# Optimization experiments

Measured on AMD Instinct MI355X. Metric: run time of the kernel, lower is better.

## Reference

```python
import jax, jax.numpy as jnp
import numpy as np

N_NODES, N_EDGES, B, L = 20000, 320000, 64, 48
EMB, OUT, HEADS, HID = 256, 64, 4, 512
S_DIM, R_DIM = 64, 64
TIME_NUM, CAT_NUM = 48, 201


def lrelu(x, s=0.2):
    return jnp.where(x >= 0, x, s * x)


def gru_cell(x, h, Wi, Wh, bi, bh):
    # PyTorch GRUCell math
    gi = x @ Wi.T + bi
    gh = h @ Wh.T + bh
    ir, iz, ig = jnp.split(gi, 3, axis=-1)
    hr, hz, hg = jnp.split(gh, 3, axis=-1)
    r = jax.nn.sigmoid(ir + hr)
    z = jax.nn.sigmoid(iz + hz)
    n = jnp.tanh(ig + r * hg)
    return (1.0 - z) * n + z * h


def gru_seq(x, Wi, Wh, bi, bh, reverse=False):
    # x: [B,L,D] -> [B,L,H]
    xs = jnp.swapaxes(x, 0, 1)
    if reverse:
        xs = xs[::-1]
    h0 = jnp.zeros((x.shape[0], Wh.shape[1]), x.dtype)

    def step(h, xt):
        h2 = gru_cell(xt, h, Wi, Wh, bi, bh)
        return h2, h2

    _, ys = jax.lax.scan(step, h0, xs)
    if reverse:
        ys = ys[::-1]
    return jnp.swapaxes(ys, 0, 1)


def setup_inputs() -> dict:
    key = jax.random.key(0)
    ks = iter(jax.random.split(key, 64))
    f32 = jnp.float32

    def rn(shape, s=0.1):
        return (s * jax.random.normal(next(ks), shape)).astype(f32)

    inp = {
        'graph_x': jnp.arange(N_NODES),
        'edge_index': jax.random.randint(next(ks), (2, N_EDGES), 0, N_NODES),
        'edge_attr': jax.random.uniform(next(ks), (N_EDGES,), f32),
        'batch_x': jax.random.randint(next(ks), (B, L), 0, N_NODES),
        'batch_time': jax.random.randint(next(ks), (B, L), 0, TIME_NUM),
        'batch_cat': jax.random.randint(next(ks), (B, L), 0, CAT_NUM),
        'poi_time': jax.random.randint(next(ks), (N_NODES,), 0, TIME_NUM),
        'poi_cat': jax.random.randint(next(ks), (N_NODES,), 0, CAT_NUM),
        # params
        'node_emb': rn((N_NODES, EMB), 1.0),
        'W_gat': rn((EMB, HEADS * OUT), 0.05),
        'att_src': rn((HEADS, OUT), 0.05),
        'att_dst': rn((HEADS, OUT), 0.05),
        'gat_bias': rn((HEADS * OUT,)),
        'time_table': rn((TIME_NUM, EMB), 1.0),
        'cat_table': rn((CAT_NUM, EMB), 1.0),
        'W_w': rn((EMB, 3 * EMB)), 'b_w': rn((EMB,)),
        'Wi_f': rn((3 * HID, EMB), 0.05), 'Wh_f': rn((3 * HID, HID), 0.05),
        'bi_f': jnp.zeros((3 * HID,), f32), 'bh_f': jnp.zeros((3 * HID,), f32),
        'Wi_bw': rn((3 * HID, EMB), 0.05), 'Wh_bw': rn((3 * HID, HID), 0.05),
        'bi_bw': jnp.zeros((3 * HID,), f32), 'bh_bw': jnp.zeros((3 * HID,), f32),
        'Wi_u': rn((3 * HID, 2 * HID), 0.05), 'Wh_u': rn((3 * HID, HID), 0.05),
        'bi_u': jnp.zeros((3 * HID,), f32), 'bh_u': jnp.zeros((3 * HID,), f32),
        'Ws_m': rn((S_DIM, 2 * HID)), 'bs_m': rn((S_DIM,)),
        'Ws_lv': rn((S_DIM, 2 * HID)), 'bs_lv': rn((S_DIM,)),
        'Wr_m': rn((R_DIM, HID)), 'br_m': rn((R_DIM,)),
        'Wr_lv': rn((R_DIM, HID)), 'br_lv': rn((R_DIM,)),
        'Wp1_i': rn((3 * HID, R_DIM), 0.05), 'Wp1_h': rn((3 * HID, HID), 0.05),
        'bp1_i': jnp.zeros((3 * HID,), f32), 'bp1_h': jnp.zeros((3 * HID,), f32),
        'Wp2_i': rn((3 * HID, HID), 0.05), 'Wp2_h': rn((3 * HID, HID), 0.05),
        'bp2_i': jnp.zeros((3 * HID,), f32), 'bp2_h': jnp.zeros((3 * HID,), f32),
        'Wpm': rn((R_DIM, HID)), 'bpm': rn((R_DIM,)),
        'Wplv': rn((R_DIM, HID)), 'bplv': rn((R_DIM,)),
        'Wd': rn((N_NODES, S_DIM + R_DIM)), 'bd': rn((N_NODES,)),
    }
    return inp


def forward(graph_x, edge_index, edge_attr, batch_x, batch_time, batch_cat,
            poi_time, poi_cat, node_emb, W_gat, att_src, att_dst, gat_bias,
            time_table, cat_table, W_w, b_w, Wi_f, Wh_f, bi_f, bh_f,
            Wi_bw, Wh_bw, bi_bw, bh_bw, Wi_u, Wh_u, bi_u, bh_u,
            Ws_m, bs_m, Ws_lv, bs_lv, Wr_m, br_m, Wr_lv, br_lv,
            Wp1_i, Wp1_h, bp1_i, bp1_h, Wp2_i, Wp2_h, bp2_i, bp2_h,
            Wpm, bpm, Wplv, bplv, Wd, bd):
    Bn, Ln = batch_x.shape
    N = node_emb.shape[0]
    heads, C = att_src.shape

    # --- weighted GAT layer over the POI graph ---
    h = node_emb[graph_x]                                   # [N, EMB]
    xW = (h @ W_gat).reshape(N, heads, C)                   # [N, H, C]
    src, dst = edge_index[0], edge_index[1]
    e = lrelu((xW * att_src).sum(-1)[src] + (xW * att_dst).sum(-1)[dst])  # [E, H]
    emax = jax.ops.segment_max(e, dst, num_segments=N)
    a = jnp.exp(e - emax[dst])
    asum = jax.ops.segment_sum(a, dst, num_segments=N)
    att = a / (asum[dst] + 1e-16)
    msg = (att * edge_attr[:, None])[:, :, None] * xW[src]  # [E, H, C]
    p = jax.ops.segment_sum(msg, dst, num_segments=N).reshape(N, heads * C) + gat_bias

    # --- per-step feature build ---
    p_h = p[batch_x]                                        # [B, L, EMB]
    t_e = time_table[batch_time]
    c_e = cat_table[batch_cat]
    ph = jnp.concatenate([p_h, t_e, c_e], axis=2) @ W_w.T + b_w  # [B, L, EMB]

    # --- posterior encode: biGRU -> s, uniGRU -> r ---
    f_fwd = gru_seq(ph, Wi_f, Wh_f, bi_f, bh_f)
    f_bwd = gru_seq(ph, Wi_bw, Wh_bw, bi_bw, bh_bw, reverse=True)
    features = jnp.concatenate([f_fwd, f_bwd], axis=2)      # [B, L, 2H]
    Hh = Wh_f.shape[1]
    frontal = features[:, Ln - 1, :Hh]
    backward = features[:, 0, Hh:2 * Hh]
    g = jnp.concatenate([frontal, backward], axis=1)
    s_mean = lrelu(g @ Ws_m.T + bs_m)
    s_logvar = lrelu(g @ Ws_lv.T + bs_lv)

    key = jax.random.key(42)
    k1, k2, k3 = jax.random.split(key, 3)
    s_post = s_mean + jax.random.normal(k1, s_mean.shape, s_mean.dtype) * jnp.exp(0.5 * s_logvar)

    r_feat = gru_seq(features, Wi_u, Wh_u, bi_u, bh_u)      # [B, L, H]
    r_mean = r_feat @ Wr_m.T + br_m
    r_logvar = r_feat @ Wr_lv.T + br_lv
    r_post = r_mean + jax.random.normal(k2, r_mean.shape, r_mean.dtype) * jnp.exp(0.5 * r_logvar)

    # --- prior: 2-layer GRUCell unroll fed with shifted r_post ---
    Rd = r_post.shape[2]
    r_in = jnp.concatenate([jnp.zeros((Bn, 1, Rd), r_post.dtype), r_post[:, :-1]], axis=1)
    r_in_t = jnp.swapaxes(r_in, 0, 1)                       # [L, B, R]
    eps = jax.random.normal(k3, (Ln, Bn, Rd), r_post.dtype)

    def pstep(carry, xe):
        h1, h2 = carry
        rt, ep = xe
        h1 = gru_cell(rt, h1, Wp1_i, Wp1_h, bp1_i, bp1_h)
        h2 = gru_cell(h1, h2, Wp2_i, Wp2_h, bp2_i, bp2_h)
        mt = h2 @ Wpm.T + bpm
        lvt = h2 @ Wplv.T + bplv
        rp = mt + ep * jnp.exp(0.5 * lvt)
        return (h1, h2), (mt, lvt, rp)

    h10 = jnp.zeros((Bn, Hh), r_post.dtype)
    h20 = jnp.zeros((Bn, Hh), r_post.dtype)
    _, (ms, lvs, rps) = jax.lax.scan(pstep, (h10, h20), (r_in_t, eps))
    r_mean_prior = jnp.swapaxes(ms, 0, 1)
    r_logvar_prior = jnp.swapaxes(lvs, 0, 1)
    r_prior = jnp.swapaxes(rps, 0, 1)

    # --- decode ---
    s_expand = jnp.broadcast_to(s_post[:, None, :], (Bn, Ln, s_post.shape[1]))
    zf = jnp.concatenate([r_post, s_expand], axis=2)
    recon_x = zf @ Wd.T + bd                                # [B, L, node_num]
    return (s_mean, s_logvar, s_post, r_mean, r_logvar, r_post,
            r_mean_prior, r_logvar_prior, r_prior, recon_x)


def reference(graph_x, edge_index, edge_attr, batch_x, batch_time, batch_cat,
              poi_time, poi_cat, node_emb, W_gat, att_src, att_dst, gat_bias,
              time_table, cat_table, W_w, b_w, Wi_f, Wh_f, bi_f, bh_f,
              Wi_bw, Wh_bw, bi_bw, bh_bw, Wi_u, Wh_u, bi_u, bh_u,
              Ws_m, bs_m, Ws_lv, bs_lv, Wr_m, br_m, Wr_lv, br_lv,
              Wp1_i, Wp1_h, bp1_i, bp1_h, Wp2_i, Wp2_h, bp2_i, bp2_h,
              Wpm, bpm, Wplv, bplv, Wd, bd):
    return forward(graph_x, edge_index, edge_attr, batch_x, batch_time, batch_cat,
                   poi_time, poi_cat, node_emb, W_gat, att_src, att_dst, gat_bias,
                   time_table, cat_table, W_w, b_w, Wi_f, Wh_f, bi_f, bh_f,
                   Wi_bw, Wh_bw, bi_bw, bh_bw, Wi_u, Wh_u, bi_u, bh_u,
                   Ws_m, bs_m, Ws_lv, bs_lv, Wr_m, br_m, Wr_lv, br_lv,
                   Wp1_i, Wp1_h, bp1_i, bp1_h, Wp2_i, Wp2_h, bp2_i, bp2_h,
                   Wpm, bpm, Wplv, bplv, Wd, bd)
```

## Files before the change

kernel.cpp:

```cpp
#include <hip/hip_runtime.h>
#include <stdint.h>
#include <stddef.h>

#define DEV __device__ __forceinline__

typedef float f32x4 __attribute__((ext_vector_type(4)));

__host__ __device__ inline void tf2x32(uint32_t k0, uint32_t k1,
                                       uint32_t x0, uint32_t x1,
                                       uint32_t* o0, uint32_t* o1) {
  uint32_t ks2 = k0 ^ k1 ^ 0x1BD11BDAu;
  uint32_t ks[3] = {k0, k1, ks2};
  x0 += k0; x1 += k1;
  const uint32_t R[8] = {13u,15u,26u,6u,17u,29u,16u,24u};
  for (int r = 0; r < 5; ++r) {
    const uint32_t* rot = (r & 1) ? (R + 4) : R;
    for (int i = 0; i < 4; ++i) {
      x0 += x1;
      uint32_t d = rot[i];
      x1 = (x1 << d) | (x1 >> (32u - d));
      x1 ^= x0;
    }
    x0 += ks[(r + 1) % 3];
    x1 += ks[(r + 2) % 3] + (uint32_t)(r + 1);
  }
  *o0 = x0; *o1 = x1;
}

DEV float erfinv_approx(float x) {
  float w = -logf((1.0f - x) * (1.0f + x));
  float p;
  if (w < 5.0f) {
    w = w - 2.5f;
    p = 2.81022636e-08f;
    p = fmaf(p, w, 3.43273939e-07f);
    p = fmaf(p, w, -3.5233877e-06f);
    p = fmaf(p, w, -4.39150654e-06f);
    p = fmaf(p, w, 0.00021858087f);
    p = fmaf(p, w, -0.00125372503f);
    p = fmaf(p, w, -0.00417768164f);
    p = fmaf(p, w, 0.246640727f);
    p = fmaf(p, w, 1.50140941f);
  } else {
    w = sqrtf(w) - 3.0f;
    p = -0.000200214257f;
    p = fmaf(p, w, 0.000100950558f);
    p = fmaf(p, w, 0.00134934322f);
    p = fmaf(p, w, -0.00367342844f);
    p = fmaf(p, w, 0.00573950773f);
    p = fmaf(p, w, -0.0076224613f);
    p = fmaf(p, w, 0.00943887047f);
    p = fmaf(p, w, 1.00167406f);
    p = fmaf(p, w, 2.83297682f);
  }
  return p * x;
}

DEV float normal_part(uint32_t ka, uint32_t kb, uint32_t idx) {
  uint32_t b1, b2;
  tf2x32(ka, kb, 0u, idx, &b1, &b2);
  uint32_t bits = b1 ^ b2;
  float f = __uint_as_float((bits >> 9) | 0x3f800000u) - 1.0f;
  const float lo = -0.99999994f;
  float u = f * 2.0f + lo;
  u = fmaxf(lo, u);
  return 1.41421356f * erfinv_approx(u);
}

DEV float lrelu(float x) { return x >= 0.f ? x : 0.2f * x; }
DEV float sigm(float x) { return 1.0f / (1.0f + expf(-x)); }

DEV float gru_out(float ir, float iz, float ig, float hr, float hz, float hg, float hprev) {
  float r = sigm(ir + hr);
  float z = sigm(iz + hz);
  float n = tanhf(ig + r * hg);
  return (1.0f - z) * n + z * hprev;
}

DEV float dot4f(float4 a, float4 b, float acc) {
  return fmaf(a.x, b.x, fmaf(a.y, b.y, fmaf(a.z, b.z, fmaf(a.w, b.w, acc))));
}

template <int K4>
DEV void dot2(const float* __restrict__ h, const float* __restrict__ w0,
              const float* __restrict__ w1, float& a0, float& a1) {
  const float4* h4 = (const float4*)h;
  const float4* p0 = (const float4*)w0;
  const float4* p1 = (const float4*)w1;
  #pragma unroll 4
  for (int k = 0; k < K4; ++k) {
    float4 hv = h4[k];
    float4 v0 = p0[k], v1 = p1[k];
    a0 = dot4f(hv, v0, a0);
    a1 = dot4f(hv, v1, a1);
  }
}

template <int K4>
DEV void dotT3p(const float* __restrict__ hp, int b,
                const float* __restrict__ w0, const float* __restrict__ w1,
                const float* __restrict__ w2, float& a0, float& a1, float& a2) {
  const float4* __restrict__ w04 = (const float4*)w0;
  const float4* __restrict__ w14 = (const float4*)w1;
  const float4* __restrict__ w24 = (const float4*)w2;
  const float4* __restrict__ h4 = (const float4*)hp;
  #pragma unroll
  for (int k4 = 0; k4 < K4; ++k4) {
    float4 hv = h4[k4 * 64 + b];
    a0 = dot4f(w04[k4], hv, a0);
    a1 = dot4f(w14[k4], hv, a1);
    a2 = dot4f(w24[k4], hv, a2);
  }
}

template <int K4>
DEV void dotT3_lds(const float* __restrict__ hl, int b,
                   const float* __restrict__ w0, const float* __restrict__ w1,
                   const float* __restrict__ w2, float& a0, float& a1, float& a2) {
  const float4* __restrict__ h4 = (const float4*)hl;
  const float4* __restrict__ w04 = (const float4*)w0;
  const float4* __restrict__ w14 = (const float4*)w1;
  const float4* __restrict__ w24 = (const float4*)w2;
  #pragma unroll 8
  for (int k4 = 0; k4 < K4; ++k4) {
    float4 hv = h4[k4 * 64 + b];
    a0 = dot4f(w04[k4], hv, a0);
    a1 = dot4f(w14[k4], hv, a1);
    a2 = dot4f(w24[k4], hv, a2);
  }
}

template <int N16>
DEV void stage_lds(float* __restrict__ dst, const float* __restrict__ src) {
  const float4* __restrict__ s4 = (const float4*)src;
  float4* __restrict__ d4 = (float4*)dst;
  int tid = threadIdx.x;
  constexpr int CH = (N16 < 16) ? N16 : 16;
  #pragma unroll
  for (int r = 0; r < N16; r += CH) {
    float4 v[CH];
    #pragma unroll
    for (int u = 0; u < CH; ++u) v[u] = s4[(size_t)(r + u) * 256 + tid];
    #pragma unroll
    for (int u = 0; u < CH; ++u) d4[(size_t)(r + u) * 256 + tid] = v[u];
  }
}

DEV size_t pk(int k, int b) { return (size_t)(k >> 2) * 256 + b * 4 + (k & 3); }

DEV void coh_store_i(int* p, int v) {
  asm volatile("global_store_dword %0, %1, off sc0 sc1" :: "v"(p), "v"(v) : "memory");
}
DEV void coh_store_f(float* p, float v) {
  asm volatile("global_store_dword %0, %1, off sc0 sc1" :: "v"(p), "v"(v) : "memory");
}
DEV void coh_store_f4(float* p, f32x4 v) {
  asm volatile("global_store_dwordx4 %0, %1, off sc0 sc1" :: "v"(p), "v"(v) : "memory");
}
DEV int coh_load_i(const int* p) {
  int v;
  asm volatile("global_load_dword %0, %1, off sc0 sc1\n\ts_waitcnt vmcnt(0)"
               : "=v"(v) : "v"(p) : "memory");
  return v;
}

DEV void flag_barrier(int* __restrict__ flags, int nblk, int myidx, int gen) {
  asm volatile("s_waitcnt vmcnt(0)" ::: "memory");
  __syncthreads();
  if (threadIdx.x == 0) coh_store_i(flags + myidx, gen);
  if ((int)threadIdx.x < nblk) {
    int spins = 0;
    while (coh_load_i(flags + threadIdx.x) < gen) {
      __builtin_amdgcn_s_sleep(2);
      if (++spins > (1 << 22)) break;
    }
  }
  __syncthreads();
}

DEV void wait_group(const int* __restrict__ flags, int nblk, int thr) {
  if ((int)threadIdx.x < nblk) {
    int spins = 0;
    while (coh_load_i(flags + threadIdx.x) < thr) {
      __builtin_amdgcn_s_sleep(2);
      if (++spins > (1 << 22)) break;
    }
  }
  __syncthreads();
}

DEV void store_packed_tile4(float* dst_t, const float (*smem)[64], int j0) {
  if (threadIdx.x < 64) {
    int bb = threadIdx.x;
    f32x4 v;
    v.x = smem[0][bb];
    v.y = smem[1][bb];
    v.z = smem[2][bb];
    v.w = smem[3][bb];
    coh_store_f4(dst_t + (size_t)(j0 >> 2) * 256 + bb * 4, v);
  }
}

#define GBM 128
#define GBN 128
#define GBK 16

__global__ __launch_bounds__(256) void gemm_nt(
    const float* __restrict__ A, const float* __restrict__ Bt,
    const float* __restrict__ bias, float* __restrict__ C,
    int M, int N, int K, const int* __restrict__ gatherA, int trGI) {
  __shared__ float As[GBK][GBM + 4];
  __shared__ float Bs[GBK][GBN + 4];
  const int bm = blockIdx.y * GBM;
  const int bn = blockIdx.x * GBN;
  const int tid = threadIdx.x;
  const int tx = tid & 15;
  const int ty = tid >> 4;
  float acc[8][8];
  #pragma unroll
  for (int i = 0; i < 8; ++i)
    #pragma unroll
    for (int j = 0; j < 8; ++j) acc[i][j] = 0.f;

  for (int k0 = 0; k0 < K; k0 += GBK) {
    #pragma unroll
    for (int s = 0; s < 2; ++s) {
      int f = tid + s * 256;
      int r = f >> 2, kq = f & 3;
      int row = bm + r;
      float4 v = make_float4(0.f, 0.f, 0.f, 0.f);
      if (row < M) {
        int ar = gatherA ? gatherA[row] : row;
        v = *(const float4*)&A[(size_t)ar * K + k0 + kq * 4];
      }
      As[kq * 4 + 0][r] = v.x;
      As[kq * 4 + 1][r] = v.y;
      As[kq * 4 + 2][r] = v.z;
      As[kq * 4 + 3][r] = v.w;
    }
    #pragma unroll
    for (int s = 0; s < 2; ++s) {
      int f = tid + s * 256;
      int r = f >> 2, kq = f & 3;
      int col = bn + r;
      float4 v = make_float4(0.f, 0.f, 0.f, 0.f);
      if (col < N) v = *(const float4*)&Bt[(size_t)col * K + k0 + kq * 4];
      Bs[kq * 4 + 0][r] = v.x;
      Bs[kq * 4 + 1][r] = v.y;
      Bs[kq * 4 + 2][r] = v.z;
      Bs[kq * 4 + 3][r] = v.w;
    }
    __syncthreads();
    #pragma unroll
    for (int kk = 0; kk < GBK; ++kk) {
      float4 a0 = *(const float4*)&As[kk][ty * 4];
      float4 a1 = *(const float4*)&As[kk][64 + ty * 4];
      float4 b0 = *(const float4*)&Bs[kk][tx * 4];
      float4 b1 = *(const float4*)&Bs[kk][64 + tx * 4];
      float av[8] = {a0.x, a0.y, a0.z, a0.w, a1.x, a1.y, a1.z, a1.w};
      float bv[8] = {b0.x, b0.y, b0.z, b0.w, b1.x, b1.y, b1.z, b1.w};
      #pragma unroll
      for (int i = 0; i < 8; ++i)
        #pragma unroll
        for (int j = 0; j < 8; ++j)
          acc[i][j] = fmaf(av[i], bv[j], acc[i][j]);
    }
    __syncthreads();
  }
  #pragma unroll
  for (int i = 0; i < 8; ++i) {
    int row = bm + ((i < 4) ? (ty * 4 + i) : (64 + ty * 4 + i - 4));
    if (row >= M) continue;
    if (trGI) {
      #pragma unroll
      for (int j = 0; j < 8; ++j) {
        int col = bn + ((j < 4) ? (tx * 4 + j) : (64 + tx * 4 + j - 4));
        if (col >= N) continue;
        float v = acc[i][j] + (bias ? bias[col] : 0.f);
        int bb = row / 48, tt = row - bb * 48;
        C[((size_t)tt * N + col) * 64 + bb] = v;
      }
    } else {
      #pragma unroll
      for (int g = 0; g < 2; ++g) {
        int col0 = bn + g * 64 + tx * 4;
        if (col0 + 3 >= N) continue;
        float4 v;
        v.x = acc[i][g * 4 + 0] + (bias ? bias[col0 + 0] : 0.f);
        v.y = acc[i][g * 4 + 1] + (bias ? bias[col0 + 1] : 0.f);
        v.z = acc[i][g * 4 + 2] + (bias ? bias[col0 + 2] : 0.f);
        v.w = acc[i][g * 4 + 3] + (bias ? bias[col0 + 3] : 0.f);
        *(float4*)&C[(size_t)row * N + col0] = v;
      }
    }
  }
}

__global__ void k_transpose(const float* __restrict__ W, float* __restrict__ Wt,
                            int rows, int cols) {
  int idx = blockIdx.x * 256 + threadIdx.x;
  if (idx >= rows * cols) return;
  int r = idx / cols, c = idx % cols;
  Wt[(size_t)c * rows + r] = W[idx];
}

__global__ void k_count_deg(const int* __restrict__ dst, int* __restrict__ deg, int nE) {
  int e = blockIdx.x * 256 + threadIdx.x;
  if (e < nE) atomicAdd(&deg[dst[e]], 1);
}

__global__ __launch_bounds__(1024) void k_scan(const int* __restrict__ deg,
                                               int* __restrict__ off,
                                               int* __restrict__ cursor, int n) {
  __shared__ int tmp[1024];
  __shared__ int carry_s;
  if (threadIdx.x == 0) carry_s = 0;
  __syncthreads();
  for (int base = 0; base < n; base += 1024) {
    int i = base + (int)threadIdx.x;
    int v = (i < n) ? deg[i] : 0;
    tmp[threadIdx.x] = v;
    __syncthreads();
    for (int s = 1; s < 1024; s <<= 1) {
      int t = (threadIdx.x >= (unsigned)s) ? tmp[threadIdx.x - s] : 0;
      __syncthreads();
      tmp[threadIdx.x] += t;
      __syncthreads();
    }
    int incl = tmp[threadIdx.x];
    int base_c = carry_s;
    int excl = incl - v;
    if (i < n) { off[i] = base_c + excl; cursor[i] = base_c + excl; }
    __syncthreads();
    if (threadIdx.x == 1023) carry_s = base_c + incl;
    __syncthreads();
  }
  if (threadIdx.x == 0) off[n] = carry_s;
}

__global__ void k_scatter(const int* __restrict__ dst, int* __restrict__ cursor,
                          int* __restrict__ csr, int nE) {
  int e = blockIdx.x * 256 + threadIdx.x;
  if (e < nE) {
    int pos = atomicAdd(&cursor[dst[e]], 1);
    csr[pos] = e;
  }
}

__global__ void k_alpha(const float* __restrict__ xW, const float* __restrict__ att_src,
                        const float* __restrict__ att_dst, float* __restrict__ as_,
                        float* __restrict__ ad_) {
  int i = blockIdx.x * 256 + threadIdx.x;
  if (i >= 80000) return;
  int n = i >> 2, h = i & 3;
  const float* xr = xW + (size_t)n * 256 + h * 64;
  const float* s = att_src + h * 64;
  const float* d = att_dst + h * 64;
  float a = 0.f, b = 0.f;
  dot2<16>(xr, s, d, a, b);
  as_[i] = a;
  ad_[i] = b;
}

__global__ __launch_bounds__(256) void k_gat_node(
    const float* __restrict__ xW, const float* __restrict__ as_,
    const float* __restrict__ ad_, const int* __restrict__ off,
    const int* __restrict__ csr, const int* __restrict__ esrc,
    const float* __restrict__ eattr, const float* __restrict__ gat_bias,
    float* __restrict__ p) {
  int n = blockIdx.x;
  int h = threadIdx.x >> 6;
  int c = threadIdx.x & 63;
  int s0 = off[n], s1 = off[n + 1];
  float adn = ad_[n * 4 + h];
  float m = -3.0e38f;
  for (int idx = s0; idx < s1; ++idx) {
    int e = csr[idx];
    int s = esrc[e];
    float ev = lrelu(as_[s * 4 + h] + adn);
    m = fmaxf(m, ev);
  }
  float sum = 0.f;
  for (int idx = s0; idx < s1; ++idx) {
    int e = csr[idx];
    int s = esrc[e];
    float ev = lrelu(as_[s * 4 + h] + adn);
    sum += expf(ev - m);
  }
  float acc = 0.f;
  for (int idx = s0; idx < s1; ++idx) {
    int e = csr[idx];
    int s = esrc[e];
    float ev = lrelu(as_[s * 4 + h] + adn);
    float w = expf(ev - m) / (sum + 1e-16f) * eattr[e];
    acc = fmaf(w, xW[(size_t)s * 256 + h * 64 + c], acc);
  }
  p[(size_t)n * 256 + h * 64 + c] = acc + gat_bias[h * 64 + c];
}

__global__ void k_build_X(const float* __restrict__ p, const float* __restrict__ tt,
                          const float* __restrict__ ct, const int* __restrict__ bx,
                          const int* __restrict__ btm, const int* __restrict__ bct,
                          float* __restrict__ X) {
  int idx = blockIdx.x * 256 + threadIdx.x;
  if (idx >= 3072 * 768) return;
  int rl = idx / 768, c = idx % 768;
  float v;
  if (c < 256) v = p[(size_t)bx[rl] * 256 + c];
  else if (c < 512) v = tt[(size_t)btm[rl] * 256 + (c - 256)];
  else v = ct[(size_t)bct[rl] * 256 + (c - 512)];
  X[idx] = v;
}


__global__ __launch_bounds__(256, 1) void k_gru_bidir_fused(
    const float* __restrict__ giT_f, const float* __restrict__ giT_b,
    const float* __restrict__ Wh_f, const float* __restrict__ bh_f,
    const float* __restrict__ Wh_b, const float* __restrict__ bh_b,
    float* __restrict__ features, float* __restrict__ hTb,
    int* __restrict__ flags) {
  __shared__ float lds_h[32768];
  __shared__ float smem[4][64];
  int w = threadIdx.x >> 6;
  int b = threadIdx.x & 63;
  int slot = blockIdx.x * 4 + w;
  int dir = slot >> 9;
  int j = slot & 511;
  int j0 = (blockIdx.x * 4) & 511;
  int gbid = blockIdx.x & 127;
  int* gflags = flags + dir * 128;
  const float* Wh = dir ? Wh_b : Wh_f;
  const float* bh = dir ? bh_b : bh_f;
  const float* gi = dir ? giT_b : giT_f;
  const float* w0 = Wh + (size_t)j * 512;
  const float* w1 = Wh + (size_t)(512 + j) * 512;
  const float* w2 = Wh + (size_t)(1024 + j) * 512;
  float bhr = bh[j], bhz = bh[512 + j], bhg = bh[1024 + j];
  float* hD = hTb + (size_t)dir * 48 * 32768;
  for (int s = 0; s < 48; ++s) {
    int t = dir ? (47 - s) : s;
    const float* gir = gi + (size_t)t * 98304;
    float giv0 = gir[j * 64 + b];
    float giv1 = gir[(512 + j) * 64 + b];
    float giv2 = gir[(1024 + j) * 64 + b];
    float hr = bhr, hz = bhz, hg = bhg, hprev = 0.f;
    if (s > 0) {
      int tp = dir ? (t + 1) : (t - 1);
      stage_lds<32>(lds_h, hD + (size_t)tp * 32768);
      __syncthreads();
      dotT3_lds<128>(lds_h, b, w0, w1, w2, hr, hz, hg);
      hprev = lds_h[pk(j, b)];
    }
    float hnew = gru_out(giv0, giv1, giv2, hr, hz, hg, hprev);
    smem[w][b] = hnew;
    features[((size_t)(b * 48 + t)) * 1024 + dir * 512 + j] = hnew;
    __syncthreads();
    store_packed_tile4(hD + (size_t)t * 32768, smem, j0);
    flag_barrier(gflags, 128, gbid, s + 1);
  }
}

__global__ __launch_bounds__(256, 1) void k_gru_u_fused(
    const float* __restrict__ giT, const float* __restrict__ Wh,
    const float* __restrict__ bh, float* __restrict__ r_feat,
    float* __restrict__ hU, int* __restrict__ flags) {
  __shared__ float lds_h[32768];
  __shared__ float smem[4][64];
  int w = threadIdx.x >> 6;
  int b = threadIdx.x & 63;
  int j = blockIdx.x * 4 + w;
  int j0 = blockIdx.x * 4;
  const float* w0 = Wh + (size_t)j * 512;
  const float* w1 = Wh + (size_t)(512 + j) * 512;
  const float* w2 = Wh + (size_t)(1024 + j) * 512;
  float bhr = bh[j], bhz = bh[512 + j], bhg = bh[1024 + j];
  for (int s = 0; s < 48; ++s) {
    const float* gir = giT + (size_t)s * 98304;
    float giv0 = gir[j * 64 + b];
    float giv1 = gir[(512 + j) * 64 + b];
    float giv2 = gir[(1024 + j) * 64 + b];
    float hr = bhr, hz = bhz, hg = bhg, hprev = 0.f;
    if (s > 0) {
      stage_lds<32>(lds_h, hU + (size_t)(s - 1) * 32768);
      __syncthreads();
      dotT3_lds<128>(lds_h, b, w0, w1, w2, hr, hz, hg);
      hprev = lds_h[pk(j, b)];
    }
    float hnew = gru_out(giv0, giv1, giv2, hr, hz, hg, hprev);
    smem[w][b] = hnew;
    r_feat[((size_t)(b * 48 + s)) * 512 + j] = hnew;
    __syncthreads();
    store_packed_tile4(hU + (size_t)s * 32768, smem, j0);
    flag_barrier(flags, 128, blockIdx.x, s + 1);
  }
}

__global__ __launch_bounds__(256, 1) void k_prior_fused(
    const float* __restrict__ r_post,
    const float* __restrict__ Wp1_i, const float* __restrict__ Wp1_h,
    const float* __restrict__ bp1_i, const float* __restrict__ bp1_h,
    const float* __restrict__ Wp2_i, const float* __restrict__ Wp2_h,
    const float* __restrict__ bp2_i, const float* __restrict__ bp2_h,
    float* __restrict__ h1S, float* __restrict__ h2S,
    float* __restrict__ rT, int* __restrict__ flags) {
  __shared__ float lds_h[32768];
  __shared__ float smem[4][64];
  int w = threadIdx.x >> 6;
  int b = threadIdx.x & 63;
  int cell = blockIdx.x >> 7;
  int gbid = blockIdx.x & 127;
  int slot = blockIdx.x * 4 + w;
  int j = slot & 511;
  int j0 = (blockIdx.x * 4) & 511;
  int* flagsA = flags;
  int* flagsB = flags + 128;

  if (cell == 0) {
    int tid = gbid * 256 + threadIdx.x;
    for (int x = tid; x < 48 * 64 * 64; x += 32768) {
      int b0 = x & 63;
      int i0 = (x >> 6) & 63;
      int t0 = x >> 12;
      coh_store_f(rT + (size_t)t0 * 4096 + pk(i0, b0),
                  r_post[((size_t)(b0 * 48 + t0)) * 64 + i0]);
    }
    flag_barrier(flagsA, 128, gbid, 1);

    const float* wi0 = Wp1_i + (size_t)j * 64;
    const float* wi1 = Wp1_i + (size_t)(512 + j) * 64;
    const float* wi2 = Wp1_i + (size_t)(1024 + j) * 64;
    const float* wh0 = Wp1_h + (size_t)j * 512;
    const float* wh1 = Wp1_h + (size_t)(512 + j) * 512;
    const float* wh2 = Wp1_h + (size_t)(1024 + j) * 512;
    float bir = bp1_i[j], biz = bp1_i[512 + j], big = bp1_i[1024 + j];
    float bhr = bp1_h[j], bhz = bp1_h[512 + j], bhg = bp1_h[1024 + j];
    for (int k = 0; k < 48; ++k) {
      float ir = bir, iz = biz, ig = big;
      float hr = bhr, hz = bhz, hg = bhg, hprev = 0.f;
      if (k > 0) {
        stage_lds<32>(lds_h, h1S + (size_t)(k - 1) * 32768);
        dotT3p<16>(rT + (size_t)(k - 1) * 4096, b, wi0, wi1, wi2, ir, iz, ig);
        __syncthreads();
        dotT3_lds<128>(lds_h, b, wh0, wh1, wh2, hr, hz, hg);
        hprev = lds_h[pk(j, b)];
      }
      smem[w][b] = gru_out(ir, iz, ig, hr, hz, hg, hprev);
      __syncthreads();
      store_packed_tile4(h1S + (size_t)k * 32768, smem, j0);
      flag_barrier(flagsA, 128, gbid, k + 2);
    }
  } else {
    const float* wi0 = Wp2_i + (size_t)j * 512;
    const float* wi1 = Wp2_i + (size_t)(512 + j) * 512;
    const float* wi2 = Wp2_i + (size_t)(1024 + j) * 512;
    const float* wh0 = Wp2_h + (size_t)j * 512;
    const float* wh1 = Wp2_h + (size_t)(512 + j) * 512;
    const float* wh2 = Wp2_h + (size_t)(1024 + j) * 512;
    float bir = bp2_i[j], biz = bp2_i[512 + j], big = bp2_i[1024 + j];
    float bhr = bp2_h[j], bhz = bp2_h[512 + j], bhg = bp2_h[1024 + j];
    for (int t = 0; t < 48; ++t) {
      wait_group(flagsA, 128, t + 2);
      stage_lds<32>(lds_h, h1S + (size_t)t * 32768);
      __syncthreads();
      float ir = bir, iz = biz, ig = big;
      dotT3_lds<128>(lds_h, b, wi0, wi1, wi2, ir, iz, ig);
      float hr = bhr, hz = bhz, hg = bhg, hprev = 0.f;
      if (t > 0) {
        __syncthreads();
        stage_lds<32>(lds_h, h2S + (size_t)(t - 1) * 32768);
        __syncthreads();
        dotT3_lds<128>(lds_h, b, wh0, wh1, wh2, hr, hz, hg);
        hprev = lds_h[pk(j, b)];
      }
      smem[w][b] = gru_out(ir, iz, ig, hr, hz, hg, hprev);
      __syncthreads();
      store_packed_tile4(h2S + (size_t)t * 32768, smem, j0);
      flag_barrier(flagsB, 128, gbid, t + 1);
    }
  }
}

__global__ void k_s_head(const float* __restrict__ features,
                         const float* __restrict__ Ws_m, const float* __restrict__ bs_m,
                         const float* __restrict__ Ws_lv, const float* __restrict__ bs_lv,
                         float* __restrict__ out, uint32_t ka, uint32_t kb) {
  int idx = blockIdx.x * 256 + threadIdx.x;
  if (idx >= 4096) return;
  int i = idx & 63, b = idx >> 6;
  const float* fr = features + ((size_t)(b * 48 + 47)) * 1024;
  const float* bk = features + ((size_t)(b * 48 + 0)) * 1024 + 512;
  const float* wm = Ws_m + (size_t)i * 1024;
  const float* wl = Ws_lv + (size_t)i * 1024;
  float m = 0.f, lv = 0.f;
  dot2<128>(fr, wm, wl, m, lv);
  dot2<128>(bk, wm + 512, wl + 512, m, lv);
  m = lrelu(m + bs_m[i]);
  lv = lrelu(lv + bs_lv[i]);
  float nz = normal_part(ka, kb, (uint32_t)idx);
  out[idx] = m;
  out[4096 + idx] = lv;
  out[8192 + idx] = m + nz * expf(0.5f * lv);
}

__global__ void k_r_head(const float* __restrict__ r_feat,
                         const float* __restrict__ Wr_m, const float* __restrict__ br_m,
                         const float* __restrict__ Wr_lv, const float* __restrict__ br_lv,
                         float* __restrict__ out, uint32_t ka, uint32_t kb) {
  int idx = blockIdx.x * 256 + threadIdx.x;
  if (idx >= 196608) return;
  int i = idx & 63;
  int bt = idx >> 6;
  const float* f = r_feat + (size_t)bt * 512;
  float m = 0.f, lv = 0.f;
  dot2<128>(f, Wr_m + (size_t)i * 512, Wr_lv + (size_t)i * 512, m, lv);
  m += br_m[i];
  lv += br_lv[i];
  float nz = normal_part(ka, kb, (uint32_t)idx);
  out[12288 + idx] = m;
  out[208896 + idx] = lv;
  out[405504 + idx] = m + nz * expf(0.5f * lv);
}

__global__ void k_prior_out(const float* __restrict__ h2S,
                            const float* __restrict__ Wpm, const float* __restrict__ bpm,
                            const float* __restrict__ Wplv, const float* __restrict__ bplv,
                            float* __restrict__ out, uint32_t ka, uint32_t kb) {
  int idx = blockIdx.x * 256 + threadIdx.x;
  if (idx >= 196608) return;
  int i = idx & 63;
  int bt = idx >> 6;
  int b = bt & 63;
  int t = bt >> 6;
  const float4* h4 = (const float4*)(h2S + (size_t)t * 32768);
  const float4* wm4 = (const float4*)(Wpm + (size_t)i * 512);
  const float4* wl4 = (const float4*)(Wplv + (size_t)i * 512);
  float m = 0.f, lv = 0.f;
  #pragma unroll 8
  for (int k4 = 0; k4 < 128; ++k4) {
    float4 hv = h4[k4 * 64 + b];
    m = dot4f(wm4[k4], hv, m);
    lv = dot4f(wl4[k4], hv, lv);
  }
  m += bpm[i];
  lv += bplv[i];
  float ep = normal_part(ka, kb, (uint32_t)idx);
  float rp = m + ep * expf(0.5f * lv);
  size_t o = ((size_t)b * 48 + t) * 64 + i;
  out[602112 + o] = m;
  out[798720 + o] = lv;
  out[995328 + o] = rp;
}

__global__ void k_build_zf(const float* __restrict__ out, float* __restrict__ zf) {
  int idx = blockIdx.x * 256 + threadIdx.x;
  if (idx >= 3072 * 128) return;
  int row = idx >> 7, c = idx & 127;
  float v;
  if (c < 64) v = out[405504 + row * 64 + c];
  else v = out[8192 + (row / 48) * 64 + (c - 64)];
  zf[idx] = v;
}

extern "C" void kernel_launch(void* const* d_in, const int* in_sizes, int n_in,
                              void* d_out, int out_size, void* d_ws, size_t ws_size,
                              hipStream_t stream) {
  const int* graph_x = (const int*)d_in[0];
  const int* edge_index = (const int*)d_in[1];
  const float* edge_attr = (const float*)d_in[2];
  const int* batch_x = (const int*)d_in[3];
  const int* batch_time = (const int*)d_in[4];
  const int* batch_cat = (const int*)d_in[5];
  const float* node_emb = (const float*)d_in[8];
  const float* W_gat = (const float*)d_in[9];
  const float* att_src = (const float*)d_in[10];
  const float* att_dst = (const float*)d_in[11];
  const float* gat_bias = (const float*)d_in[12];
  const float* time_table = (const float*)d_in[13];
  const float* cat_table = (const float*)d_in[14];
  const float* W_w = (const float*)d_in[15];
  const float* b_w = (const float*)d_in[16];
  const float* Wi_f = (const float*)d_in[17];
  const float* Wh_f = (const float*)d_in[18];
  const float* bi_f = (const float*)d_in[19];
  const float* bh_f = (const float*)d_in[20];
  const float* Wi_bw = (const float*)d_in[21];
  const float* Wh_bw = (const float*)d_in[22];
  const float* bi_bw = (const float*)d_in[23];
  const float* bh_bw = (const float*)d_in[24];
  const float* Wi_u = (const float*)d_in[25];
  const float* Wh_u = (const float*)d_in[26];
  const float* bi_u = (const float*)d_in[27];
  const float* bh_u = (const float*)d_in[28];
  const float* Ws_m = (const float*)d_in[29];
  const float* bs_m = (const float*)d_in[30];
  const float* Ws_lv = (const float*)d_in[31];
  const float* bs_lv = (const float*)d_in[32];
  const float* Wr_m = (const float*)d_in[33];
  const float* br_m = (const float*)d_in[34];
  const float* Wr_lv = (const float*)d_in[35];
  const float* br_lv = (const float*)d_in[36];
  const float* Wp1_i = (const float*)d_in[37];
  const float* Wp1_h = (const float*)d_in[38];
  const float* bp1_i = (const float*)d_in[39];
  const float* bp1_h = (const float*)d_in[40];
  const float* Wp2_i = (const float*)d_in[41];
  const float* Wp2_h = (const float*)d_in[42];
  const float* bp2_i = (const float*)d_in[43];
  const float* bp2_h = (const float*)d_in[44];
  const float* Wpm = (const float*)d_in[45];
  const float* bpm = (const float*)d_in[46];
  const float* Wplv = (const float*)d_in[47];
  const float* bplv = (const float*)d_in[48];
  const float* Wd = (const float*)d_in[49];
  const float* bd = (const float*)d_in[50];
  float* out = (float*)d_out;

  uint32_t k1a, k1b, k2a, k2b, k3a, k3b;
  tf2x32(0u, 42u, 0u, 0u, &k1a, &k1b);
  tf2x32(0u, 42u, 0u, 1u, &k2a, &k2b);
  tf2x32(0u, 42u, 0u, 2u, &k3a, &k3b);

  float* ws = (float*)d_ws;
  size_t o = 0;
  auto alloc = [&](size_t n) { float* q = ws + o; o += n; return q; };
  float* R1 = alloc(5120000);
  float* R2 = alloc(5120000);
  float* R3 = alloc(4718592);
  float* R4 = alloc(786432);
  float* as_ = alloc(80000);
  float* ad_ = alloc(80000);
  float* Wgt = alloc(65536);
  int* deg = (int*)alloc(20000);
  int* off = (int*)alloc(20001);
  int* cursor = (int*)alloc(20000);
  int* csr = (int*)alloc(320000);
  float* rT = alloc(196608);
  int* flags = (int*)alloc(768);

  float* xW = R1;
  float* features = R1;
  float* r_feat = R1 + 3145728;
  float* p = R2;
  float* giT_b = R2;
  float* hU = R2;
  float* X = R3;
  float* giT_f = R3;
  float* giT_u = R3;
  float* h1S = R3;
  float* h2S = R3 + 1572864;
  float* ph = R4;
  float* zf = R4;
  float* hTb = out + 1191936;

  const int* esrc = edge_index;
  const int* edst = edge_index + 320000;

  dim3 B(256);

  (void)hipMemsetAsync(deg, 0, 20000 * sizeof(int), stream);
  (void)hipMemsetAsync(flags, 0, 768 * sizeof(int), stream);

  k_transpose<<<dim3(256), B, 0, stream>>>(W_gat, Wgt, 256, 256);
  k_count_deg<<<dim3(1250), B, 0, stream>>>(edst, deg, 320000);
  k_scan<<<dim3(1), dim3(1024), 0, stream>>>(deg, off, cursor, 20000);
  k_scatter<<<dim3(1250), B, 0, stream>>>(edst, cursor, csr, 320000);
  gemm_nt<<<dim3(2, 157), B, 0, stream>>>(node_emb, Wgt, nullptr, xW,
                                          20000, 256, 256, graph_x, 0);
  k_alpha<<<dim3(313), B, 0, stream>>>(xW, att_src, att_dst, as_, ad_);
  k_gat_node<<<dim3(20000), B, 0, stream>>>(xW, as_, ad_, off, csr, esrc,
                                            edge_attr, gat_bias, p);

  k_build_X<<<dim3(9216), B, 0, stream>>>(p, time_table, cat_table, batch_x,
                                          batch_time, batch_cat, X);
  gemm_nt<<<dim3(2, 24), B, 0, stream>>>(X, W_w, b_w, ph, 3072, 256, 768,
                                         nullptr, 0);

  gemm_nt<<<dim3(12, 24), B, 0, stream>>>(ph, Wi_f, bi_f, giT_f, 3072, 1536, 256,
                                          nullptr, 1);
  gemm_nt<<<dim3(12, 24), B, 0, stream>>>(ph, Wi_bw, bi_bw, giT_b, 3072, 1536, 256,
                                          nullptr, 1);
  k_gru_bidir_fused<<<dim3(256), B, 0, stream>>>(
      giT_f, giT_b, Wh_f, bh_f, Wh_bw, bh_bw, features, hTb, flags);

  k_s_head<<<dim3(16), B, 0, stream>>>(features, Ws_m, bs_m, Ws_lv, bs_lv,
                                       out, k1a, k1b);

  gemm_nt<<<dim3(12, 24), B, 0, stream>>>(features, Wi_u, bi_u, giT_u,
                                          3072, 1536, 1024, nullptr, 1);
  k_gru_u_fused<<<dim3(128), B, 0, stream>>>(giT_u, Wh_u, bh_u, r_feat,
                                             hU, flags + 256);

  k_r_head<<<dim3(768), B, 0, stream>>>(r_feat, Wr_m, br_m, Wr_lv, br_lv,
                                        out, k2a, k2b);

  k_prior_fused<<<dim3(256), B, 0, stream>>>(
      out + 405504, Wp1_i, Wp1_h, bp1_i, bp1_h, Wp2_i, Wp2_h, bp2_i, bp2_h,
      h1S, h2S, rT, flags + 384);
  k_prior_out<<<dim3(768), B, 0, stream>>>(h2S, Wpm, bpm, Wplv, bplv,
                                           out, k3a, k3b);

  k_build_zf<<<dim3(1536), B, 0, stream>>>(out, zf);
  gemm_nt<<<dim3(157, 24), B, 0, stream>>>(zf, Wd, bd, out + 1191936,
                                           3072, 20000, 128, nullptr, 0);
}
```

Measured before the change: 5.108 ms.

## Restructure prior GRU kernel into batch-grouped tiles with group-local flag barriers

The two-cell prior GRU kernel is rewritten. Each block now handles 32 hidden units by 4 batch rows, with the K reduction split across two halves and combined through shared memory. Each block stages only a 4-row hidden tile instead of the full 64x512 state, and the grid-wide barrier over 128 blocks becomes a barrier among 16 blocks that share a batch group. The r_post transpose moves into a separate pre-kernel, and the output head reads the new batch-major layout. The intent is to cut LDS staging cost and barrier latency per timestep and to allow two blocks per CU. The cost is that weights are re-read by 16 batch groups and there are more per-step syncthreads.

```diff
diff --git a/kernel.cpp b/kernel.cpp
--- a/kernel.cpp
+++ b/kernel.cpp
@@ -97,23 +97,6 @@
 }
 
 template <int K4>
-DEV void dotT3p(const float* __restrict__ hp, int b,
-                const float* __restrict__ w0, const float* __restrict__ w1,
-                const float* __restrict__ w2, float& a0, float& a1, float& a2) {
-  const float4* __restrict__ w04 = (const float4*)w0;
-  const float4* __restrict__ w14 = (const float4*)w1;
-  const float4* __restrict__ w24 = (const float4*)w2;
-  const float4* __restrict__ h4 = (const float4*)hp;
-  #pragma unroll
-  for (int k4 = 0; k4 < K4; ++k4) {
-    float4 hv = h4[k4 * 64 + b];
-    a0 = dot4f(w04[k4], hv, a0);
-    a1 = dot4f(w14[k4], hv, a1);
-    a2 = dot4f(w24[k4], hv, a2);
-  }
-}
-
-template <int K4>
 DEV void dotT3_lds(const float* __restrict__ hl, int b,
                    const float* __restrict__ w0, const float* __restrict__ w1,
                    const float* __restrict__ w2, float& a0, float& a1, float& a2) {
@@ -411,7 +394,6 @@
   else v = ct[(size_t)bct[rl] * 256 + (c - 512)];
   X[idx] = v;
 }
-
 
 __global__ __launch_bounds__(256, 1) void k_gru_bidir_fused(
     const float* __restrict__ giT_f, const float* __restrict__ giT_b,
@@ -495,87 +477,162 @@
   }
 }
 
-__global__ __launch_bounds__(256, 1) void k_prior_fused(
-    const float* __restrict__ r_post,
+
+__global__ void k_prior_pre(const float* __restrict__ r_post,
+                            float* __restrict__ rTP) {
+  int idx = blockIdx.x * 256 + threadIdx.x;
+  if (idx >= 196608) return;
+  int i = idx & 63;
+  int rest = idx >> 6;
+  int bl = rest & 3;
+  int bg = (rest >> 2) & 15;
+  int t = rest >> 6;
+  rTP[idx] = r_post[((size_t)((bg * 4 + bl) * 48 + t)) * 64 + i];
+}
+
+__global__ __launch_bounds__(256, 2) void k_prior2(
+    const float* __restrict__ rTP,
     const float* __restrict__ Wp1_i, const float* __restrict__ Wp1_h,
     const float* __restrict__ bp1_i, const float* __restrict__ bp1_h,
     const float* __restrict__ Wp2_i, const float* __restrict__ Wp2_h,
     const float* __restrict__ bp2_i, const float* __restrict__ bp2_h,
-    float* __restrict__ h1S, float* __restrict__ h2S,
-    float* __restrict__ rT, int* __restrict__ flags) {
-  __shared__ float lds_h[32768];
-  __shared__ float smem[4][64];
-  int w = threadIdx.x >> 6;
-  int b = threadIdx.x & 63;
-  int cell = blockIdx.x >> 7;
-  int gbid = blockIdx.x & 127;
-  int slot = blockIdx.x * 4 + w;
-  int j = slot & 511;
-  int j0 = (blockIdx.x * 4) & 511;
+    float* __restrict__ h1P, float* __restrict__ h2P,
+    int* __restrict__ flags) {
+  __shared__ float lds_h[4][512];
+  __shared__ float part_i[2][128][3];
+  __shared__ float part_h[2][128][3];
+  int bid = blockIdx.x;
+  int cell = bid >> 8;
+  int lid = bid & 255;
+  int jg = lid >> 4, bg = lid & 15;
+  int tid = threadIdx.x;
+  int half = tid >> 7;
+  int c = tid & 127;
+  int jl = c & 31;
+  int bl = c >> 5;
+  int j = jg * 32 + jl;
   int* flagsA = flags;
-  int* flagsB = flags + 128;
+  int* flagsB = flags + 256;
+  float4* d4 = (float4*)&lds_h[0][0];
 
   if (cell == 0) {
-    int tid = gbid * 256 + threadIdx.x;
-    for (int x = tid; x < 48 * 64 * 64; x += 32768) {
-      int b0 = x & 63;
-      int i0 = (x >> 6) & 63;
-      int t0 = x >> 12;
-      coh_store_f(rT + (size_t)t0 * 4096 + pk(i0, b0),
-                  r_post[((size_t)(b0 * 48 + t0)) * 64 + i0]);
-    }
-    flag_barrier(flagsA, 128, gbid, 1);
-
-    const float* wi0 = Wp1_i + (size_t)j * 64;
-    const float* wi1 = Wp1_i + (size_t)(512 + j) * 64;
-    const float* wi2 = Wp1_i + (size_t)(1024 + j) * 64;
-    const float* wh0 = Wp1_h + (size_t)j * 512;
-    const float* wh1 = Wp1_h + (size_t)(512 + j) * 512;
-    const float* wh2 = Wp1_h + (size_t)(1024 + j) * 512;
-    float bir = bp1_i[j], biz = bp1_i[512 + j], big = bp1_i[1024 + j];
-    float bhr = bp1_h[j], bhz = bp1_h[512 + j], bhg = bp1_h[1024 + j];
+    const float4* wi0 = (const float4*)(Wp1_i + (size_t)j * 64);
+    const float4* wi1 = (const float4*)(Wp1_i + (size_t)(512 + j) * 64);
+    const float4* wi2 = (const float4*)(Wp1_i + (size_t)(1024 + j) * 64);
+    const float4* wh0 = (const float4*)(Wp1_h + (size_t)j * 512);
+    const float4* wh1 = (const float4*)(Wp1_h + (size_t)(512 + j) * 512);
+    const float4* wh2 = (const float4*)(Wp1_h + (size_t)(1024 + j) * 512);
     for (int k = 0; k < 48; ++k) {
-      float ir = bir, iz = biz, ig = big;
-      float hr = bhr, hz = bhz, hg = bhg, hprev = 0.f;
       if (k > 0) {
-        stage_lds<32>(lds_h, h1S + (size_t)(k - 1) * 32768);
-        dotT3p<16>(rT + (size_t)(k - 1) * 4096, b, wi0, wi1, wi2, ir, iz, ig);
+        const float4* s4 = (const float4*)(h1P + ((size_t)(k - 1) * 16 + bg) * 2048);
+        d4[tid] = s4[tid];
+        d4[tid + 256] = s4[tid + 256];
         __syncthreads();
-        dotT3_lds<128>(lds_h, b, wh0, wh1, wh2, hr, hz, hg);
-        hprev = lds_h[pk(j, b)];
+        const float4* h4 = (const float4*)&lds_h[bl][0];
+        float a0 = 0.f, a1 = 0.f, a2 = 0.f;
+        #pragma unroll 8
+        for (int q = 0; q < 64; ++q) {
+          int k4 = half * 64 + q;
+          float4 hv = h4[k4];
+          a0 = dot4f(wh0[k4], hv, a0);
+          a1 = dot4f(wh1[k4], hv, a1);
+          a2 = dot4f(wh2[k4], hv, a2);
+        }
+        part_h[half][c][0] = a0; part_h[half][c][1] = a1; part_h[half][c][2] = a2;
+        const float4* r4 =
+            (const float4*)(rTP + (((size_t)(k - 1) * 16 + bg) * 4 + bl) * 64);
+        float b0 = 0.f, b1 = 0.f, b2 = 0.f;
+        #pragma unroll
+        for (int q = 0; q < 8; ++q) {
+          int k4 = half * 8 + q;
+          float4 rv = r4[k4];
+          b0 = dot4f(wi0[k4], rv, b0);
+          b1 = dot4f(wi1[k4], rv, b1);
+          b2 = dot4f(wi2[k4], rv, b2);
+        }
+        part_i[half][c][0] = b0; part_i[half][c][1] = b1; part_i[half][c][2] = b2;
+        __syncthreads();
       }
-      smem[w][b] = gru_out(ir, iz, ig, hr, hz, hg, hprev);
+      if (tid < 128) {
+        int cc = tid, jl2 = cc & 31, bl2 = cc >> 5;
+        int jj = jg * 32 + jl2;
+        float ir = bp1_i[jj], iz = bp1_i[512 + jj], ig = bp1_i[1024 + jj];
+        float hr = bp1_h[jj], hz = bp1_h[512 + jj], hg = bp1_h[1024 + jj];
+        float hp = 0.f;
+        if (k > 0) {
+          ir += part_i[0][cc][0] + part_i[1][cc][0];
+          iz += part_i[0][cc][1] + part_i[1][cc][1];
+          ig += part_i[0][cc][2] + part_i[1][cc][2];
+          hr += part_h[0][cc][0] + part_h[1][cc][0];
+          hz += part_h[0][cc][1] + part_h[1][cc][1];
+          hg += part_h[0][cc][2] + part_h[1][cc][2];
+          hp = lds_h[bl2][jj];
+        }
+        coh_store_f(h1P + ((size_t)k * 16 + bg) * 2048 + bl2 * 512 + jj,
+                    gru_out(ir, iz, ig, hr, hz, hg, hp));
+      }
+      flag_barrier(flagsA + bg * 16, 16, jg, k + 1);
+    }
+  } else {
+    const float4* wi0 = (const float4*)(Wp2_i + (size_t)j * 512);
+    const float4* wi1 = (const float4*)(Wp2_i + (size_t)(512 + j) * 512);
+    const float4* wi2 = (const float4*)(Wp2_i + (size_t)(1024 + j) * 512);
+    const float4* wh0 = (const float4*)(Wp2_h + (size_t)j * 512);
+    const float4* wh1 = (const float4*)(Wp2_h + (size_t)(512 + j) * 512);
+    const float4* wh2 = (const float4*)(Wp2_h + (size_t)(1024 + j) * 512);
+    for (int t = 0; t < 48; ++t) {
+      wait_group(flagsA + bg * 16, 16, t + 1);
+      const float4* s4 = (const float4*)(h1P + ((size_t)t * 16 + bg) * 2048);
+      d4[tid] = s4[tid];
+      d4[tid + 256] = s4[tid + 256];
       __syncthreads();
-      store_packed_tile4(h1S + (size_t)k * 32768, smem, j0);
-      flag_barrier(flagsA, 128, gbid, k + 2);
-    }
-  } else {
-    const float* wi0 = Wp2_i + (size_t)j * 512;
-    const float* wi1 = Wp2_i + (size_t)(512 + j) * 512;
-    const float* wi2 = Wp2_i + (size_t)(1024 + j) * 512;
-    const float* wh0 = Wp2_h + (size_t)j * 512;
-    const float* wh1 = Wp2_h + (size_t)(512 + j) * 512;
-    const float* wh2 = Wp2_h + (size_t)(1024 + j) * 512;
-    float bir = bp2_i[j], biz = bp2_i[512 + j], big = bp2_i[1024 + j];
-    float bhr = bp2_h[j], bhz = bp2_h[512 + j], bhg = bp2_h[1024 + j];
-    for (int t = 0; t < 48; ++t) {
-      wait_group(flagsA, 128, t + 2);
-      stage_lds<32>(lds_h, h1S + (size_t)t * 32768);
+      const float4* h4 = (const float4*)&lds_h[bl][0];
+      float b0 = 0.f, b1 = 0.f, b2 = 0.f;
+      #pragma unroll 8
+      for (int q = 0; q < 64; ++q) {
+        int k4 = half * 64 + q;
+        float4 hv = h4[k4];
+        b0 = dot4f(wi0[k4], hv, b0);
+        b1 = dot4f(wi1[k4], hv, b1);
+        b2 = dot4f(wi2[k4], hv, b2);
+      }
+      part_i[half][c][0] = b0; part_i[half][c][1] = b1; part_i[half][c][2] = b2;
       __syncthreads();
-      float ir = bir, iz = biz, ig = big;
-      dotT3_lds<128>(lds_h, b, wi0, wi1, wi2, ir, iz, ig);
-      float hr = bhr, hz = bhz, hg = bhg, hprev = 0.f;
       if (t > 0) {
+        const float4* s4b = (const float4*)(h2P + ((size_t)(t - 1) * 16 + bg) * 2048);
+        d4[tid] = s4b[tid];
+        d4[tid + 256] = s4b[tid + 256];
         __syncthreads();
-        stage_lds<32>(lds_h, h2S + (size_t)(t - 1) * 32768);
+        float a0 = 0.f, a1 = 0.f, a2 = 0.f;
+        #pragma unroll 8
+        for (int q = 0; q < 64; ++q) {
+          int k4 = half * 64 + q;
+          float4 hv = h4[k4];
+          a0 = dot4f(wh0[k4], hv, a0);
+          a1 = dot4f(wh1[k4], hv, a1);
+          a2 = dot4f(wh2[k4], hv, a2);
+        }
+        part_h[half][c][0] = a0; part_h[half][c][1] = a1; part_h[half][c][2] = a2;
         __syncthreads();
-        dotT3_lds<128>(lds_h, b, wh0, wh1, wh2, hr, hz, hg);
-        hprev = lds_h[pk(j, b)];
       }
-      smem[w][b] = gru_out(ir, iz, ig, hr, hz, hg, hprev);
-      __syncthreads();
-      store_packed_tile4(h2S + (size_t)t * 32768, smem, j0);
-      flag_barrier(flagsB, 128, gbid, t + 1);
+      if (tid < 128) {
+        int cc = tid, jl2 = cc & 31, bl2 = cc >> 5;
+        int jj = jg * 32 + jl2;
+        float ir = part_i[0][cc][0] + part_i[1][cc][0] + bp2_i[jj];
+        float iz = part_i[0][cc][1] + part_i[1][cc][1] + bp2_i[512 + jj];
+        float ig = part_i[0][cc][2] + part_i[1][cc][2] + bp2_i[1024 + jj];
+        float hr = bp2_h[jj], hz = bp2_h[512 + jj], hg = bp2_h[1024 + jj];
+        float hp = 0.f;
+        if (t > 0) {
+          hr += part_h[0][cc][0] + part_h[1][cc][0];
+          hz += part_h[0][cc][1] + part_h[1][cc][1];
+          hg += part_h[0][cc][2] + part_h[1][cc][2];
+          hp = lds_h[bl2][jj];
+        }
+        coh_store_f(h2P + ((size_t)t * 16 + bg) * 2048 + bl2 * 512 + jj,
+                    gru_out(ir, iz, ig, hr, hz, hg, hp));
+      }
+      flag_barrier(flagsB + bg * 16, 16, jg, t + 1);
     }
   }
 }
@@ -621,7 +678,7 @@
   out[405504 + idx] = m + nz * expf(0.5f * lv);
 }
 
-__global__ void k_prior_out(const float* __restrict__ h2S,
+__global__ void k_prior_out(const float* __restrict__ h2P,
                             const float* __restrict__ Wpm, const float* __restrict__ bpm,
                             const float* __restrict__ Wplv, const float* __restrict__ bplv,
                             float* __restrict__ out, uint32_t ka, uint32_t kb) {
@@ -631,13 +688,14 @@
   int bt = idx >> 6;
   int b = bt & 63;
   int t = bt >> 6;
-  const float4* h4 = (const float4*)(h2S + (size_t)t * 32768);
+  const float4* h4 =
+      (const float4*)(h2P + (((size_t)t * 16 + (b >> 2)) * 4 + (b & 3)) * 512);
   const float4* wm4 = (const float4*)(Wpm + (size_t)i * 512);
   const float4* wl4 = (const float4*)(Wplv + (size_t)i * 512);
   float m = 0.f, lv = 0.f;
   #pragma unroll 8
   for (int k4 = 0; k4 < 128; ++k4) {
-    float4 hv = h4[k4 * 64 + b];
+    float4 hv = h4[k4];
     m = dot4f(wm4[k4], hv, m);
     lv = dot4f(wl4[k4], hv, lv);
   }
@@ -734,8 +792,8 @@
   int* off = (int*)alloc(20001);
   int* cursor = (int*)alloc(20000);
   int* csr = (int*)alloc(320000);
-  float* rT = alloc(196608);
-  int* flags = (int*)alloc(768);
+  float* rTP = alloc(196608);
+  int* flags = (int*)alloc(1024);
 
   float* xW = R1;
   float* features = R1;
@@ -746,8 +804,8 @@
   float* X = R3;
   float* giT_f = R3;
   float* giT_u = R3;
-  float* h1S = R3;
-  float* h2S = R3 + 1572864;
+  float* h1P = R3;
+  float* h2P = R3 + 1572864;
   float* ph = R4;
   float* zf = R4;
   float* hTb = out + 1191936;
@@ -758,7 +816,7 @@
   dim3 B(256);
 
   (void)hipMemsetAsync(deg, 0, 20000 * sizeof(int), stream);
-  (void)hipMemsetAsync(flags, 0, 768 * sizeof(int), stream);
+  (void)hipMemsetAsync(flags, 0, 1024 * sizeof(int), stream);
 
   k_transpose<<<dim3(256), B, 0, stream>>>(W_gat, Wgt, 256, 256);
   k_count_deg<<<dim3(1250), B, 0, stream>>>(edst, deg, 320000);
@@ -793,10 +851,11 @@
   k_r_head<<<dim3(768), B, 0, stream>>>(r_feat, Wr_m, br_m, Wr_lv, br_lv,
                                         out, k2a, k2b);
 
-  k_prior_fused<<<dim3(256), B, 0, stream>>>(
-      out + 405504, Wp1_i, Wp1_h, bp1_i, bp1_h, Wp2_i, Wp2_h, bp2_i, bp2_h,
-      h1S, h2S, rT, flags + 384);
-  k_prior_out<<<dim3(768), B, 0, stream>>>(h2S, Wpm, bpm, Wplv, bplv,
+  k_prior_pre<<<dim3(768), B, 0, stream>>>(out + 405504, rTP);
+  k_prior2<<<dim3(512), B, 0, stream>>>(
+      rTP, Wp1_i, Wp1_h, bp1_i, bp1_h, Wp2_i, Wp2_h, bp2_i, bp2_h,
+      h1P, h2P, flags + 384);
+  k_prior_out<<<dim3(768), B, 0, stream>>>(h2P, Wpm, bpm, Wplv, bplv,
                                            out, k3a, k3b);
 
   k_build_zf<<<dim3(1536), B, 0, stream>>>(out, zf);
```

After: 6.716 ms. 31.5% more time.
